# Kernel tuning notes

Measured on AMD Instinct MI355X. Metric: run time of the kernel, lower is better.

The kernel has to match this reference:

```python
import jax, jax.numpy as jnp
import numpy as np

N, D_IN, H1, H, D_OUT = 65536, 256, 512, 1024, 16
EPS_BN = 1e-5
EPS_COS = 1e-10


def _batchnorm(x, gamma, beta):
    # torch BatchNorm1d, training mode: batch mean, biased variance
    mu = jnp.mean(x, axis=0)
    var = jnp.var(x, axis=0)
    return (x - mu) * jax.lax.rsqrt(var + EPS_BN) * gamma + beta


def setup_inputs() -> dict:
    key = jax.random.key(0)
    ks = jax.random.split(key, 8)
    inp = {
        "x": jax.random.normal(ks[0], (N, D_IN), dtype=jnp.float32),
        # fc1 / bn1
        "W1": jax.random.normal(ks[1], (D_IN, H1), dtype=jnp.float32) * 0.05,
        "b1": jnp.zeros((H1,), jnp.float32),
        "g1": jnp.ones((H1,), jnp.float32),
        "be1": jnp.zeros((H1,), jnp.float32),
        # fc2 / bn2
        "W2": jax.random.normal(ks[2], (H1, 2 * H1), dtype=jnp.float32) * 0.05,
        "b2": jnp.zeros((2 * H1,), jnp.float32),
        "g2": jnp.ones((2 * H1,), jnp.float32),
        "be2": jnp.zeros((2 * H1,), jnp.float32),
        # fc3
        "W3": jax.random.normal(ks[3], (2 * H1, H), dtype=jnp.float32) * 0.05,
        "b3": jnp.zeros((H,), jnp.float32),
        # GCN weights (nn.Parameter(torch.randn(...)))
        "GW1": jax.random.normal(ks[4], (H, H), dtype=jnp.float32) * 0.05,
        "GW2": jax.random.normal(ks[5], (H, D_OUT), dtype=jnp.float32) * 0.05,
    }
    return inp


def _support_from_features(h):
    # cosine similarity between COLUMNS of h: [H, H]
    gram = h.T @ h                                  # [H, H]
    col_norm = jnp.sqrt(jnp.clip(jnp.diag(gram), 0.0))
    adj = gram / (col_norm[:, None] * col_norm[None, :] + EPS_COS)
    # preprocess_adj: A = adj + I, symmetric normalization D^-1/2 A D^-1/2
    A = adj + jnp.eye(H, dtype=h.dtype)
    d = jnp.sum(A, axis=1)
    d_inv_sqrt = jnp.where(d > 0, jax.lax.rsqrt(jnp.where(d > 0, d, 1.0)), 0.0)
    S = d_inv_sqrt[:, None] * A * d_inv_sqrt[None, :]
    # original builds adjacency from detached numpy -> constant wrt params
    return jax.lax.stop_gradient(S)


def reference(x, W1, b1, g1, be1, W2, b2, g2, be2, W3, b3, GW1, GW2):
    h = jax.nn.relu(_batchnorm(x @ W1 + b1, g1, be1))          # [N, H1]
    h = jax.nn.relu(_batchnorm(h @ W2 + b2, g2, be2))          # [N, 2*H1]
    h = jax.nn.relu(h @ W3 + b3)                               # [N, H]
    S = _support_from_features(h)                              # [H, H]
    out = jax.nn.relu((h @ S) @ GW1)                           # GCN layer 1 [N, H]
    out = jax.nn.relu((out @ S) @ GW2)                         # GCN layer 2 [N, D_OUT]
    return out
```

## Files before the change

### kernel.cpp

```cpp
#include <hip/hip_runtime.h>
#include <cstddef>
#include <cstdint>


typedef unsigned short u16;
typedef unsigned int   u32;
typedef __attribute__((ext_vector_type(8))) short  s16x8;
typedef __attribute__((ext_vector_type(4))) float  f32x4;

__device__ __forceinline__ float b2f(u16 u){ u32 x = ((u32)u)<<16; float f; __builtin_memcpy(&f,&x,4); return f; }
__device__ __forceinline__ u16 f2b(float f){ u32 x; __builtin_memcpy(&x,&f,4); x += 0x7fffu + ((x>>16)&1u); return (u16)(x>>16); }

typedef const __attribute__((address_space(1))) u32* gas1_t;
typedef __attribute__((address_space(3))) u32*       las3_t;
__device__ __forceinline__ void gld_lds16(const void* g, void* l){
  __builtin_amdgcn_global_load_lds((gas1_t)g, (las3_t)l, 16, 0, 0);
}

template<int EPI, int STATS>
__global__ __launch_bounds__(256)
void gemm128(const u16* __restrict__ A, const u16* __restrict__ Bt,
             void* __restrict__ Cout, const float* __restrict__ bias,
             float* __restrict__ ssum, float* __restrict__ ssq,
             int ksz, int lda, int ldb, int ldc, int lgn)
{
  __shared__ u16 lAs[128*64];
  __shared__ u16 lBs[128*64];
  const int tid = threadIdx.x, wid = tid >> 6, lane = tid & 63;

  const int nwg  = gridDim.x;
  const int bid  = blockIdx.x;
  const int swz  = (bid & 7) * (nwg >> 3) + (bid >> 3);
  const int nblk = swz & ((1 << lgn) - 1);
  const int mblk = swz >> lgn;

  f32x4 acc[4][4];
#pragma unroll
  for (int i = 0; i < 4; ++i)
#pragma unroll
    for (int j = 0; j < 4; ++j) acc[i][j] = (f32x4){0.f,0.f,0.f,0.f};

  const u16* Abase = A  + (size_t)mblk*128*lda;
  const u16* Bbase = Bt + (size_t)nblk*128*ldb;
  const int wm = wid >> 1, wn = wid & 1;
  const int lr = lane & 15, lk = (lane >> 4) * 8;
  const u16* lA = &lAs[wm*64*64];
  const u16* lB = &lBs[wn*64*64];
  const int srow = tid >> 3;
  const int scol = (tid & 7) * 8;

  const int nkt = ksz >> 6;
  for (int kt = 0; kt < nkt; ++kt) {
    __syncthreads();
    const u16* Ak = Abase + kt*64;
    const u16* Bk = Bbase + kt*64;
#pragma unroll
    for (int i = 0; i < 4; ++i) {
      gld_lds16(Ak + (size_t)(i*32 + srow)*lda + scol, &lAs[i*2048 + wid*512]);
      gld_lds16(Bk + (size_t)(i*32 + srow)*ldb + scol, &lBs[i*2048 + wid*512]);
    }
    __syncthreads();
#pragma unroll
    for (int kk = 0; kk < 64; kk += 32) {
      s16x8 af[4], bf[4];
#pragma unroll
      for (int mi = 0; mi < 4; ++mi) af[mi] = *(const s16x8*)(lA + (mi*16+lr)*64 + kk + lk);
#pragma unroll
      for (int ni = 0; ni < 4; ++ni) bf[ni] = *(const s16x8*)(lB + (ni*16+lr)*64 + kk + lk);
#pragma unroll
      for (int mi = 0; mi < 4; ++mi)
#pragma unroll
        for (int ni = 0; ni < 4; ++ni)
          acc[mi][ni] = __builtin_amdgcn_mfma_f32_16x16x32_bf16(af[mi], bf[ni], acc[mi][ni], 0, 0, 0);
    }
  }

  const int r0 = mblk*128 + wm*64;
  const int c0 = nblk*128 + wn*64;
  const int rr = (lane >> 4) * 4;

  if (STATS) {
#pragma unroll
    for (int ni = 0; ni < 4; ++ni) {
      float s = 0.f, q = 0.f;
#pragma unroll
      for (int mi = 0; mi < 4; ++mi)
#pragma unroll
        for (int r = 0; r < 4; ++r) { float v = acc[mi][ni][r]; s += v; q += v*v; }
      s += __shfl_xor(s, 16, 64); q += __shfl_xor(q, 16, 64);
      s += __shfl_xor(s, 32, 64); q += __shfl_xor(q, 32, 64);
      if ((lane >> 4) == 0) {
        atomicAdd(&ssum[c0 + ni*16 + lr], s);
        atomicAdd(&ssq [c0 + ni*16 + lr], q);
      }
    }
  }

  if (EPI == 3) {
    u16* Cp = (u16*)Cout;
#pragma unroll
    for (int mi = 0; mi < 4; ++mi)
#pragma unroll
      for (int ni = 0; ni < 4; ++ni)
#pragma unroll
        for (int r = 0; r < 4; ++r)
          Cp[(size_t)(c0 + ni*16 + lr)*ldc + (r0 + mi*16 + rr + r)] = f2b(acc[mi][ni][r]);
  } else {
    u16* Cp = (u16*)Cout;
    float bv[4];
#pragma unroll
    for (int ni = 0; ni < 4; ++ni)
      bv[ni] = (EPI == 1 && bias) ? bias[c0 + ni*16 + lr] : 0.f;
#pragma unroll
    for (int mi = 0; mi < 4; ++mi)
#pragma unroll
      for (int ni = 0; ni < 4; ++ni)
#pragma unroll
        for (int r = 0; r < 4; ++r) {
          float v = acc[mi][ni][r];
          if (EPI == 1) v = fmaxf(v + bv[ni], 0.f);
          Cp[(size_t)(r0 + mi*16 + rr + r)*ldc + (c0 + ni*16 + lr)] = f2b(v);
        }
  }
}

__global__ __launch_bounds__(256)
void gram_gemm(const u16* __restrict__ T, float* __restrict__ P, int ld, int ksz)
{
  __shared__ u16 lAs[128*64];
  __shared__ u16 lBs[128*64];
  const int tid = threadIdx.x, wid = tid >> 6, lane = tid & 63;

  const int b = blockIdx.x;
  int i = (int)((sqrtf(8.f*(float)b + 1.f) - 1.f) * 0.5f);
  while ((i+1)*(i+2)/2 <= b) ++i;
  while (i*(i+1)/2 > b) --i;
  const int j = b - i*(i+1)/2;
  const int k0 = blockIdx.z * ksz;

  f32x4 acc[4][4];
#pragma unroll
  for (int a = 0; a < 4; ++a)
#pragma unroll
    for (int c = 0; c < 4; ++c) acc[a][c] = (f32x4){0.f,0.f,0.f,0.f};

  const u16* Abase = T + (size_t)i*128*ld + k0;
  const u16* Bbase = T + (size_t)j*128*ld + k0;
  const int wm = wid >> 1, wn = wid & 1;
  const int lr = lane & 15, lk = (lane >> 4) * 8;
  const u16* lA = &lAs[wm*64*64];
  const u16* lB = &lBs[wn*64*64];
  const int srow = tid >> 3;
  const int scol = (tid & 7) * 8;

  const int nkt = ksz >> 6;
  for (int kt = 0; kt < nkt; ++kt) {
    __syncthreads();
    const u16* Ak = Abase + kt*64;
    const u16* Bk = Bbase + kt*64;
#pragma unroll
    for (int t = 0; t < 4; ++t) {
      gld_lds16(Ak + (size_t)(t*32 + srow)*ld + scol, &lAs[t*2048 + wid*512]);
      gld_lds16(Bk + (size_t)(t*32 + srow)*ld + scol, &lBs[t*2048 + wid*512]);
    }
    __syncthreads();
#pragma unroll
    for (int kk = 0; kk < 64; kk += 32) {
      s16x8 af[4], bf[4];
#pragma unroll
      for (int mi = 0; mi < 4; ++mi) af[mi] = *(const s16x8*)(lA + (mi*16+lr)*64 + kk + lk);
#pragma unroll
      for (int ni = 0; ni < 4; ++ni) bf[ni] = *(const s16x8*)(lB + (ni*16+lr)*64 + kk + lk);
#pragma unroll
      for (int mi = 0; mi < 4; ++mi)
#pragma unroll
        for (int ni = 0; ni < 4; ++ni)
          acc[mi][ni] = __builtin_amdgcn_mfma_f32_16x16x32_bf16(af[mi], bf[ni], acc[mi][ni], 0, 0, 0);
    }
  }

  float* Cp = P + (size_t)blockIdx.z * 1048576ull;
  const int r0 = i*128 + wm*64;
  const int c0 = j*128 + wn*64;
  const int rr = (lane >> 4) * 4;
#pragma unroll
  for (int mi = 0; mi < 4; ++mi)
#pragma unroll
    for (int ni = 0; ni < 4; ++ni)
#pragma unroll
      for (int r = 0; r < 4; ++r) {
        size_t idx = (size_t)(r0 + mi*16 + rr + r)*1024 + (c0 + ni*16 + lr);
        Cp[idx] += acc[mi][ni][r];
      }
}


__global__ void zero_f32(float* __restrict__ p, int n)
{
  int i = blockIdx.x*256 + threadIdx.x;
  if (i < n) p[i] = 0.f;
}

__global__ void transpose_cvt(const float* __restrict__ in, u16* __restrict__ out, int R, int C)
{
  __shared__ float t[32][33];
  const int bc = blockIdx.x*32, br = blockIdx.y*32;
  const int tx = threadIdx.x & 31, ty = threadIdx.x >> 5;
#pragma unroll
  for (int i = 0; i < 4; ++i) t[ty + 8*i][tx] = in[(size_t)(br + ty + 8*i)*C + bc + tx];
  __syncthreads();
#pragma unroll
  for (int i = 0; i < 4; ++i) out[(size_t)(bc + ty + 8*i)*R + br + tx] = f2b(t[tx][ty + 8*i]);
}

__global__ void cvt_x(const float* __restrict__ in, u16* __restrict__ out, size_t n8)
{
  size_t i0 = (size_t)blockIdx.x*blockDim.x + threadIdx.x;
  size_t str = (size_t)gridDim.x*blockDim.x;
  for (size_t v = i0; v < n8; v += str) {
    const float* p = in + v*8;
    f32x4 a = *(const f32x4*)p;
    f32x4 b = *(const f32x4*)(p + 4);
    s16x8 o;
    o[0]=(short)f2b(a[0]); o[1]=(short)f2b(a[1]); o[2]=(short)f2b(a[2]); o[3]=(short)f2b(a[3]);
    o[4]=(short)f2b(b[0]); o[5]=(short)f2b(b[1]); o[6]=(short)f2b(b[2]); o[7]=(short)f2b(b[3]);
    *(s16x8*)(out + v*8) = o;
  }
}

__global__ void bn_finalize(const float* __restrict__ sum, const float* __restrict__ sumsq,
                            const float* __restrict__ g, const float* __restrict__ be,
                            float* __restrict__ a, float* __restrict__ b, int C, float invN)
{
  int c = blockIdx.x*256 + threadIdx.x;
  if (c < C) {
    float mu  = sum[c]*invN;
    float var = sumsq[c]*invN - mu*mu;
    float ac  = g[c]*rsqrtf(var + 1e-5f);
    a[c] = ac;
    b[c] = be[c] - mu*ac;
  }
}

__global__ void bn_apply(u16* __restrict__ X, const float* __restrict__ a,
                         const float* __restrict__ b, size_t n8, int cmask)
{
  size_t i0 = (size_t)blockIdx.x*blockDim.x + threadIdx.x;
  size_t str = (size_t)gridDim.x*blockDim.x;
  for (size_t v = i0; v < n8; v += str) {
    size_t base = v*8;
    int c0 = (int)(base & (size_t)cmask);
    s16x8 x = *(const s16x8*)(X + base);
    s16x8 y;
#pragma unroll
    for (int j = 0; j < 8; ++j) {
      float f = b2f((u16)x[j]) * a[c0 + j] + b[c0 + j];
      y[j] = (short)f2b(fmaxf(f, 0.f));
    }
    *(s16x8*)(X + base) = y;
  }
}

__global__ void transpose_bf16(const u16* __restrict__ in, u16* __restrict__ out, int R, int C)
{
  __shared__ u16 t[64][72];
  const int r0 = blockIdx.x*64, c0 = blockIdx.y*64;
  const int tid = threadIdx.x;
#pragma unroll
  for (int i = 0; i < 2; ++i) {
    int v = i*256 + tid;
    int r = v >> 3, c8 = (v & 7)*8;
    *(s16x8*)&t[r][c8] = *(const s16x8*)&in[(size_t)(r0 + r)*C + c0 + c8];
  }
  __syncthreads();
#pragma unroll
  for (int i = 0; i < 2; ++i) {
    int v = i*256 + tid;
    int c = v >> 3, r8 = (v & 7)*8;
    s16x8 o;
#pragma unroll
    for (int j = 0; j < 8; ++j) o[j] = (short)t[r8 + j][c];
    *(s16x8*)&out[(size_t)(c0 + c)*R + r0 + r8] = o;
  }
}

__global__ void reduce_part(const float* __restrict__ P, float* __restrict__ G, int n, int parts)
{
  int e = blockIdx.x*256 + threadIdx.x;
  if (e < n) {
    float s = 0.f;
    for (int p = 0; p < parts; ++p) s += P[(size_t)p*n + e];
    G[e] = s;
  }
}

__global__ void mirror_up(float* __restrict__ G)
{
  int e = blockIdx.x*256 + threadIdx.x;
  int r = e >> 10, c = e & 1023;
  if (c > r) G[(size_t)r*1024 + c] = G[(size_t)c*1024 + r];
}

__global__ void k_norms(const float* __restrict__ gram, float* __restrict__ norms)
{
  int i = blockIdx.x*256 + threadIdx.x;
  if (i < 1024) norms[i] = sqrtf(fmaxf(gram[(size_t)i*1025], 0.f));
}

__global__ void k_degree(const float* __restrict__ gram, const float* __restrict__ norms,
                         float* __restrict__ dinv)
{
  const int i = blockIdx.x, t = threadIdx.x;
  const float ni = norms[i];
  float p = 0.f;
  for (int j = t; j < 1024; j += 256)
    p += gram[(size_t)i*1024 + j] / (ni*norms[j] + 1e-10f);
#pragma unroll
  for (int o = 32; o; o >>= 1) p += __shfl_down(p, o, 64);
  __shared__ float ws[4];
  if ((t & 63) == 0) ws[t >> 6] = p;
  __syncthreads();
  if (t == 0) {
    float d = ws[0] + ws[1] + ws[2] + ws[3] + 1.0f;
    dinv[i] = d > 0.f ? rsqrtf(d) : 0.f;
  }
}

__global__ void k_sbuild(const float* __restrict__ gram, const float* __restrict__ norms,
                         const float* __restrict__ dinv, u16* __restrict__ Sb)
{
  int e = blockIdx.x*256 + threadIdx.x;
  int i = e >> 10, j = e & 1023;
  float adj = gram[e] / (norms[i]*norms[j] + 1e-10f);
  float a = adj + (i == j ? 1.f : 0.f);
  Sb[e] = f2b(dinv[i]*a*dinv[j]);
}

__global__ void k_sg2t(const u16* __restrict__ SB, const float* __restrict__ GW2,
                       u16* __restrict__ SG2T)
{
  const int t = threadIdx.x;
  const int i = blockIdx.x*16 + (t >> 4);
  const int j = t & 15;
  float acc = 0.f;
  for (int m = 0; m < 1024; ++m) acc += b2f(SB[(size_t)i*1024 + m]) * GW2[m*16 + j];
  SG2T[j*1024 + i] = f2b(acc);
}

__global__ __launch_bounds__(256)
void k_final4(const u16* __restrict__ A0, const u16* __restrict__ A1,
              const u16* __restrict__ A2, const u16* __restrict__ A3,
              const u16* __restrict__ Bt, float* __restrict__ out)
{
  const int y = blockIdx.y;
  const u16* A = (y == 0) ? A0 : (y == 1) ? A1 : (y == 2) ? A2 : A3;
  float* o = out + (size_t)y * 16384 * 16;
  const int wid = threadIdx.x >> 6, lane = threadIdx.x & 63;
  const int r0 = (blockIdx.x*4 + wid) * 16;
  const int lr = lane & 15, lk = (lane >> 4)*8;
  f32x4 acc = (f32x4){0.f,0.f,0.f,0.f};
  const u16* Ab = A  + (size_t)(r0 + lr)*1024 + lk;
  const u16* Bb = Bt + (size_t)lr*1024 + lk;
#pragma unroll 4
  for (int k = 0; k < 1024; k += 32) {
    s16x8 a = *(const s16x8*)(Ab + k);
    s16x8 b = *(const s16x8*)(Bb + k);
    acc = __builtin_amdgcn_mfma_f32_16x16x32_bf16(a, b, acc, 0, 0, 0);
  }
  const int col = lane & 15;
  const int rbase = r0 + (lane >> 4)*4;
#pragma unroll
  for (int r = 0; r < 4; ++r)
    o[(size_t)(rbase + r)*16 + col] = fmaxf(acc[r], 0.f);
}


extern "C" void kernel_launch(void* const* d_in, const int* in_sizes, int n_in,
                              void* d_out, int out_size, void* d_ws, size_t ws_size,
                              hipStream_t stream)
{
  const float* x   = (const float*)d_in[0];
  const float* W1  = (const float*)d_in[1];
  const float* g1  = (const float*)d_in[3];
  const float* be1 = (const float*)d_in[4];
  const float* W2  = (const float*)d_in[5];
  const float* g2  = (const float*)d_in[7];
  const float* be2 = (const float*)d_in[8];
  const float* W3  = (const float*)d_in[9];
  const float* b3  = (const float*)d_in[10];
  const float* GW1 = (const float*)d_in[11];
  const float* GW2 = (const float*)d_in[12];
  float* outp = (float*)d_out;

  const size_t NEED_S = 215277568ull;
  if (ws_size < NEED_S) {
    zero_f32<<<4096, 256, 0, stream>>>((float*)d_out, 1048576);
    return;
  }
  char* w = (char*)d_ws;
  const size_t CHUNK = 16777216ull;
  u16*   hbuf = (u16*)(w);
  u16*   xb   = (u16*)(w);
  float* part = (float*)(w + 100663296ull);
  u16*   h1   = (u16*)(w + 134217728ull);
  u16*   tmp  = (u16*)(w + 134217728ull);
  u16*   h3t32= (u16*)(w + 167772160ull);
  char*  tail = w + 201326592ull;
  u16*   W1T  = (u16*)(tail);
  u16*   W2T  = (u16*)(tail + 262144);
  u16*   W3T  = (u16*)(tail + 1310720);
  u16*   GW1T = (u16*)(tail + 3407872);
  u16*   SB   = (u16*)(tail + 5505024);
  u16*   SG1T = (u16*)(tail + 7602176);
  u16*   SG2T = (u16*)(tail + 9699328);
  float* GRAM = (float*)(tail + 9732096);
  float* NORMS= (float*)(tail + 13926400);
  float* DINV = (float*)(tail + 13930496);
  float* BNS  = (float*)(tail + 13934592);
  float* BNQ  = (float*)(tail + 13938688);
  float* BNA  = (float*)(tail + 13942784);
  float* BNB  = (float*)(tail + 13946880);

  u16* h3c[4] = { tmp,            hbuf,  hbuf + CHUNK, hbuf + 2*CHUNK };
  u16* o1c[4] = { hbuf + 3*CHUNK, tmp,   hbuf,         hbuf + CHUNK };

  transpose_cvt<<<dim3(16, 8),  256, 0, stream>>>(W1,  W1T,  256, 512);
  transpose_cvt<<<dim3(32, 16), 256, 0, stream>>>(W2,  W2T,  512, 1024);
  transpose_cvt<<<dim3(32, 32), 256, 0, stream>>>(W3,  W3T,  1024, 1024);
  transpose_cvt<<<dim3(32, 32), 256, 0, stream>>>(GW1, GW1T, 1024, 1024);
  cvt_x<<<2048, 256, 0, stream>>>(x, xb, 2097152ull);

  zero_f32<<<8, 256, 0, stream>>>(BNS, 2048);
  gemm128<0,1><<<dim3(2048,1,1), 256, 0, stream>>>(xb, W1T, h1, nullptr,
      BNS, BNQ, 256, 256, 256, 512, 2);
  bn_finalize<<<2, 256, 0, stream>>>(BNS, BNQ, g1, be1, BNA, BNB, 512, 1.f/65536.f);
  bn_apply<<<2048, 256, 0, stream>>>(h1, BNA, BNB, 4194304ull, 511);

  zero_f32<<<8, 256, 0, stream>>>(BNS, 2048);
  gemm128<0,1><<<dim3(4096,1,1), 256, 0, stream>>>(h1, W2T, hbuf, nullptr,
      BNS, BNQ, 512, 512, 512, 1024, 3);
  bn_finalize<<<4, 256, 0, stream>>>(BNS, BNQ, g2, be2, BNA, BNB, 1024, 1.f/65536.f);
  bn_apply<<<2048, 256, 0, stream>>>(hbuf, BNA, BNB, 8388608ull, 1023);

  for (int c = 0; c < 4; ++c)
    gemm128<1,0><<<dim3(1024,1,1), 256, 0, stream>>>(
        hbuf + (size_t)c*CHUNK, W3T, h3c[c], b3, nullptr, nullptr,
        1024, 1024, 1024, 1024, 3);

  zero_f32<<<32768, 256, 0, stream>>>(part, 8388608);
  for (int c = 0; c < 4; ++c) {
    transpose_bf16<<<dim3(256, 16), 256, 0, stream>>>(h3c[c], h3t32, 16384, 1024);
    gram_gemm<<<dim3(36,1,8), 256, 0, stream>>>(h3t32, part, 16384, 2048);
  }
  reduce_part<<<4096, 256, 0, stream>>>(part, GRAM, 1048576, 8);
  mirror_up<<<4096, 256, 0, stream>>>(GRAM);

  k_norms<<<4, 256, 0, stream>>>(GRAM, NORMS);
  k_degree<<<1024, 256, 0, stream>>>(GRAM, NORMS, DINV);
  k_sbuild<<<4096, 256, 0, stream>>>(GRAM, NORMS, DINV, SB);
  k_sg2t<<<64, 256, 0, stream>>>(SB, GW2, SG2T);
  gemm128<3,0><<<dim3(64,1,1), 256, 0, stream>>>(SB, GW1T, SG1T, nullptr,
      nullptr, nullptr, 1024, 1024, 1024, 1024, 3);

  for (int c = 0; c < 4; ++c)
    gemm128<1,0><<<dim3(1024,1,1), 256, 0, stream>>>(
        h3c[c], SG1T, o1c[c], nullptr, nullptr, nullptr,
        1024, 1024, 1024, 1024, 3);

  k_final4<<<dim3(256,4), 256, 0, stream>>>(o1c[0], o1c[1], o1c[2], o1c[3],
      SG2T, outp);

  (void)in_sizes; (void)n_in; (void)out_size;
}
```

Baseline: 1.186 ms.

## Double-buffer LDS tiles in gemm128 and gram_gemm to overlap loads with MFMA

Both bf16 GEMM kernels now hold two LDS buffers for the A and B tiles. The next k-tile is issued with global_load_lds into the idle buffer while the current tile is consumed by MFMAs, and there is one barrier per iteration instead of two. The aim is to hide global memory latency behind compute. It doubles LDS use per block to 64KB, which can lower the number of resident workgroups. Overlap may also be lost if the compiler waits on outstanding vector-memory loads before the LDS reads.

```diff
diff --git a/kernel.cpp b/kernel.cpp
--- a/kernel.cpp
+++ b/kernel.cpp
@@ -24,8 +24,8 @@
              float* __restrict__ ssum, float* __restrict__ ssq,
              int ksz, int lda, int ldb, int ldc, int lgn)
 {
-  __shared__ u16 lAs[128*64];
-  __shared__ u16 lBs[128*64];
+  __shared__ u16 lAs[2][128*64];
+  __shared__ u16 lBs[2][128*64];
   const int tid = threadIdx.x, wid = tid >> 6, lane = tid & 63;
 
   const int nwg  = gridDim.x;
@@ -44,22 +44,27 @@
   const u16* Bbase = Bt + (size_t)nblk*128*ldb;
   const int wm = wid >> 1, wn = wid & 1;
   const int lr = lane & 15, lk = (lane >> 4) * 8;
-  const u16* lA = &lAs[wm*64*64];
-  const u16* lB = &lBs[wn*64*64];
   const int srow = tid >> 3;
   const int scol = (tid & 7) * 8;
 
-  const int nkt = ksz >> 6;
-  for (int kt = 0; kt < nkt; ++kt) {
-    __syncthreads();
+  auto stage = [&](int kt, int b) {
     const u16* Ak = Abase + kt*64;
     const u16* Bk = Bbase + kt*64;
 #pragma unroll
     for (int i = 0; i < 4; ++i) {
-      gld_lds16(Ak + (size_t)(i*32 + srow)*lda + scol, &lAs[i*2048 + wid*512]);
-      gld_lds16(Bk + (size_t)(i*32 + srow)*ldb + scol, &lBs[i*2048 + wid*512]);
-    }
+      gld_lds16(Ak + (size_t)(i*32 + srow)*lda + scol, &lAs[b][i*2048 + wid*512]);
+      gld_lds16(Bk + (size_t)(i*32 + srow)*ldb + scol, &lBs[b][i*2048 + wid*512]);
+    }
+  };
+
+  const int nkt = ksz >> 6;
+  stage(0, 0);
+  for (int kt = 0; kt < nkt; ++kt) {
+    const int cur = kt & 1;
     __syncthreads();
+    if (kt + 1 < nkt) stage(kt + 1, cur ^ 1);
+    const u16* lA = &lAs[cur][wm*64*64];
+    const u16* lB = &lBs[cur][wn*64*64];
 #pragma unroll
     for (int kk = 0; kk < 64; kk += 32) {
       s16x8 af[4], bf[4];
@@ -127,8 +132,8 @@
 __global__ __launch_bounds__(256)
 void gram_gemm(const u16* __restrict__ T, float* __restrict__ P, int ld, int ksz)
 {
-  __shared__ u16 lAs[128*64];
-  __shared__ u16 lBs[128*64];
+  __shared__ u16 lAs[2][128*64];
+  __shared__ u16 lBs[2][128*64];
   const int tid = threadIdx.x, wid = tid >> 6, lane = tid & 63;
 
   const int b = blockIdx.x;
@@ -148,22 +153,27 @@
   const u16* Bbase = T + (size_t)j*128*ld + k0;
   const int wm = wid >> 1, wn = wid & 1;
   const int lr = lane & 15, lk = (lane >> 4) * 8;
-  const u16* lA = &lAs[wm*64*64];
-  const u16* lB = &lBs[wn*64*64];
   const int srow = tid >> 3;
   const int scol = (tid & 7) * 8;
 
-  const int nkt = ksz >> 6;
-  for (int kt = 0; kt < nkt; ++kt) {
-    __syncthreads();
+  auto stage = [&](int kt, int bb) {
     const u16* Ak = Abase + kt*64;
     const u16* Bk = Bbase + kt*64;
 #pragma unroll
     for (int t = 0; t < 4; ++t) {
-      gld_lds16(Ak + (size_t)(t*32 + srow)*ld + scol, &lAs[t*2048 + wid*512]);
-      gld_lds16(Bk + (size_t)(t*32 + srow)*ld + scol, &lBs[t*2048 + wid*512]);
-    }
+      gld_lds16(Ak + (size_t)(t*32 + srow)*ld + scol, &lAs[bb][t*2048 + wid*512]);
+      gld_lds16(Bk + (size_t)(t*32 + srow)*ld + scol, &lBs[bb][t*2048 + wid*512]);
+    }
+  };
+
+  const int nkt = ksz >> 6;
+  stage(0, 0);
+  for (int kt = 0; kt < nkt; ++kt) {
+    const int cur = kt & 1;
     __syncthreads();
+    if (kt + 1 < nkt) stage(kt + 1, cur ^ 1);
+    const u16* lA = &lAs[cur][wm*64*64];
+    const u16* lB = &lBs[cur][wn*64*64];
 #pragma unroll
     for (int kk = 0; kk < 64; kk += 32) {
       s16x8 af[4], bf[4];
```

After: 1.170 ms. No clear change (-1.4%).
